# Kernel optimization log

Measured on AMD Instinct MI355X. Metric: run time of the kernel, lower is better.

The kernel has to match this reference:

```python
import jax, jax.numpy as jnp
import numpy as np

B, H, S, DH = 8, 16, 512, 64
HID = H * DH


def setup_inputs() -> dict:
    key = jax.random.key(0)
    ks = jax.random.split(key, 16)
    # padding vectors: 1s up to a per-sample valid length, 0s afterwards
    # (first zero index == valid length, matching create_padding_matrix semantics)
    len_q = jax.random.randint(ks[0], (B,), S // 2, S + 1)
    len_k = jax.random.randint(ks[1], (B,), S // 2, S + 1)
    r = jnp.arange(S)
    pq = (r[None, :] < len_q[:, None]).astype(jnp.int32)
    pk = (r[None, :] < len_k[:, None]).astype(jnp.int32)
    sc = 0.02
    inp = {
        "padding_vector_q": pq,
        "padding_vector_k": pk,
        "query_t_1": jnp.zeros((1,), jnp.float32),
        "key_t": jnp.zeros((1,), jnp.float32),
        "hidden_states": jnp.zeros((1,), jnp.float32),
        "hidden_states_t_1": jnp.zeros((1,), jnp.float32),
        "hidden_from_last": jax.random.normal(ks[2], (B, H, S, DH), jnp.float32),
        "hidden_current": jax.random.normal(ks[3], (B, H, S, DH), jnp.float32),
        "max_n_codes": S,
        "interpretabity": 0,
        "iter_idx": 0,
        "W_v1": jax.random.normal(ks[4], (HID, HID), jnp.float32) * sc,
        "b_v1": jnp.zeros((HID,), jnp.float32),
        "W_v": jax.random.normal(ks[5], (HID, HID), jnp.float32) * sc,
        "b_v": jnp.zeros((HID,), jnp.float32),
        "W_q": jax.random.normal(ks[6], (HID, HID), jnp.float32) * sc,
        "b_q": jnp.zeros((HID,), jnp.float32),
        "W_k": jax.random.normal(ks[7], (HID, HID), jnp.float32) * sc,
        "b_k": jnp.zeros((HID,), jnp.float32),
        "W_cat": jax.random.normal(ks[8], (2 * DH, DH), jnp.float32) * sc,
        "b_cat": jnp.zeros((DH,), jnp.float32),
    }
    return inp


def reference(padding_vector_q, padding_vector_k, query_t_1, key_t,
              hidden_states, hidden_states_t_1, hidden_from_last, hidden_current,
              max_n_codes, interpretabity, iter_idx,
              W_v1, b_v1, W_v, b_v, W_q, b_q, W_k, b_k, W_cat, b_cat):
    b, h, s, dh = hidden_from_last.shape
    hid = h * dh
    # permute(0,2,1,3).flatten(start_dim=2): [B,H,S,Dh] -> [B,S,H*Dh]
    flat_last = hidden_from_last.transpose(0, 2, 1, 3).reshape(b, s, hid)
    flat_cur = hidden_current.transpose(0, 2, 1, 3).reshape(b, s, hid)

    def heads(x):  # [B,S,HID] -> [B,H,S,Dh]
        return x.reshape(b, s, h, dh).transpose(0, 2, 1, 3)

    v1 = heads(flat_last @ W_v1 + b_v1)   # value_t_1(hidden_from_last)
    vt = heads(flat_cur @ W_v + b_v)      # value(hidden_current)
    q = heads(flat_last @ W_q + b_q)
    k = heads(flat_cur @ W_k + b_k)

    scores = jnp.einsum('bhqd,bhkd->bhqk', q, k) / jnp.sqrt(jnp.float32(dh))
    scores_t = scores.transpose(0, 1, 3, 2)  # [B,H,Sk,Sq] (original permute(0,1,3,2))

    # vectorized per-sample padding mask: valid window [0:padd_q, 0:padd_k]
    def first_zero(v):
        hz = jnp.any(v == 0, axis=1)
        return jnp.where(hz, jnp.argmax(v == 0, axis=1), s)

    pq_len = first_zero(padding_vector_q)
    pk_len = first_zero(padding_vector_k)
    r = jnp.arange(s)
    valid = (r[None, :, None] < pq_len[:, None, None]) & \
            (r[None, None, :] < pk_len[:, None, None])  # [B,S,S]
    mask = (~valid)[:, None, :, :]  # True = masked, broadcast over heads

    # -1e9 underflows to exactly 0 after softmax in fp32, matching the
    # masked_fill(-inf) -> softmax -> masked_fill(0) chain without NaN rows
    NEG = jnp.float32(-1e9)
    attn = jax.nn.softmax(jnp.where(mask, NEG, scores_t), axis=-1)
    attention_values = jnp.where(mask, jnp.float32(0), attn)

    context_layer = jnp.einsum('bhks,bhsd->bhkd', attention_values, v1)
    context_layer2 = jnp.concatenate([context_layer, vt], axis=-1) @ W_cat + b_cat
    return attention_values, scores_t, context_layer2, context_layer
```

## Files before the change

kernel.cpp:

```cpp
#include <hip/hip_runtime.h>
#include <cstddef>

#define NB 8
#define NH 16
#define NS 512
#define NDH 64
#define NHID 1024
#define NBH (NB*NH)

#define QKV_ELEMS (NB*NH*NS*NDH)
#define ATTN_ELEMS ((size_t)NB*NH*(size_t)NS*NS)

typedef __bf16 bf16;
typedef __attribute__((ext_vector_type(8))) __bf16 bf16x8;
typedef __attribute__((ext_vector_type(4))) __bf16 bf16x4;
typedef __attribute__((ext_vector_type(4))) float f32x4;
typedef unsigned int u32;

__device__ __forceinline__ void gload_lds16(const void* g, void* l) {
    __builtin_amdgcn_global_load_lds(
        (const __attribute__((address_space(1))) u32*)g,
        (__attribute__((address_space(3))) u32*)l, 16, 0, 0);
}

__device__ __forceinline__ int swz(int idx, int row) { return idx ^ ((row & 7) << 3); }

__global__ void lens_kernel(const int* __restrict__ pq, const int* __restrict__ pk,
                            int* __restrict__ lens) {
    int bi = blockIdx.x;
    const int* v = (bi < NB) ? pq : pk;
    int b = bi & (NB - 1);
    int lane = threadIdx.x;
    int local = NS;
#pragma unroll
    for (int p = 0; p < NS / 64; ++p) {
        int idx = p * 64 + lane;
        if (v[b * NS + idx] == 0 && idx < local) local = idx;
    }
#pragma unroll
    for (int m = 32; m >= 1; m >>= 1) {
        int o = __shfl_xor(local, m, 64);
        local = min(local, o);
    }
    if (lane == 0) lens[bi] = local;
}

__global__ __launch_bounds__(256) void cvtA_kernel(
    const float* __restrict__ hl, const float* __restrict__ hc,
    bf16* __restrict__ al, bf16* __restrict__ ac) {
    const float* src = blockIdx.z ? hc : hl;
    bf16* dst = blockIdx.z ? ac : al;
    int tid = blockIdx.x * 256 + threadIdx.x;
    int d8 = tid & 7, s = (tid >> 3) & 511, h = (tid >> 12) & 15, b = tid >> 16;
    const float* p = &src[(((size_t)b * NH + h) * NS + s) * NDH + d8 * 8];
    float4 v0 = *(const float4*)p;
    float4 v1 = *(const float4*)(p + 4);
    bf16x8 o;
    o[0] = (bf16)v0.x; o[1] = (bf16)v0.y; o[2] = (bf16)v0.z; o[3] = (bf16)v0.w;
    o[4] = (bf16)v1.x; o[5] = (bf16)v1.y; o[6] = (bf16)v1.z; o[7] = (bf16)v1.w;
    *(bf16x8*)&dst[((size_t)(b * NS + s)) * NHID + h * NDH + d8 * 8] = o;
}

__global__ __launch_bounds__(256) void cvtW_kernel(
    const float* __restrict__ Wq, const float* __restrict__ Wk,
    const float* __restrict__ Wv1, const float* __restrict__ Wv,
    bf16* __restrict__ Wt) {
    const float* W;
    switch (blockIdx.z) {
        case 0: W = Wq; break;
        case 1: W = Wk; break;
        case 2: W = Wv1; break;
        default: W = Wv; break;
    }
    bf16* out = Wt + (size_t)blockIdx.z * NHID * NHID;
    __shared__ bf16 T[64][72];
    int t = threadIdx.x;
    int k0 = blockIdx.y * 64, n0 = blockIdx.x * 64;
#pragma unroll
    for (int p = 0; p < 4; ++p) {
        int kk = p * 16 + (t >> 4), c4 = (t & 15) * 4;
        float4 v = *(const float4*)&W[(size_t)(k0 + kk) * NHID + n0 + c4];
        T[c4 + 0][kk] = (bf16)v.x;
        T[c4 + 1][kk] = (bf16)v.y;
        T[c4 + 2][kk] = (bf16)v.z;
        T[c4 + 3][kk] = (bf16)v.w;
    }
    __syncthreads();
#pragma unroll
    for (int p = 0; p < 2; ++p) {
        int f = p * 256 + t;
        int nn = f >> 3, k8 = (f & 7) * 8;
        bf16x8 o;
#pragma unroll
        for (int e = 0; e < 8; ++e) o[e] = T[nn][k8 + e];
        *(bf16x8*)&out[(size_t)(n0 + nn) * NHID + k0 + k8] = o;
    }
}

__global__ __launch_bounds__(256) void proj_kernel(
    const bf16* __restrict__ al, const bf16* __restrict__ ac,
    const bf16* __restrict__ Wt,
    const float* __restrict__ bq, const float* __restrict__ bk,
    const float* __restrict__ bv1, const float* __restrict__ bv,
    bf16* __restrict__ oq, bf16* __restrict__ ok,
    bf16* __restrict__ ov1, bf16* __restrict__ ovt) {
    __shared__ bf16 As[128 * 64];
    __shared__ bf16 Bs[128 * 64];
    const bf16* A; const bf16* W; const float* bias; bf16* dst;
    switch (blockIdx.z) {
        case 0: A = al; W = Wt;                 bias = bq;  dst = oq;  break;
        case 1: A = ac; W = Wt + 1048576;       bias = bk;  dst = ok;  break;
        case 2: A = al; W = Wt + 2097152;       bias = bv1; dst = ov1; break;
        default: A = ac; W = Wt + 3145728;      bias = bv;  dst = ovt; break;
    }
    int t = threadIdx.x, lane = t & 63, w = t >> 6;
    int wm = w & 1, wn = w >> 1;
    int m0 = blockIdx.y * 128, n0 = blockIdx.x * 128;
    int lrow = lane >> 3, lk8 = (lane & 7) * 8;
    f32x4 acc[4][4];
#pragma unroll
    for (int i = 0; i < 4; ++i)
#pragma unroll
        for (int j = 0; j < 4; ++j) acc[i][j] = (f32x4){0.f, 0.f, 0.f, 0.f};

    for (int kb = 0; kb < NHID; kb += 64) {
#pragma unroll
        for (int i = 0; i < 4; ++i) {
            int seg = w * 2048 + i * 512;
            int row = (w * 32 + i * 8) + lrow;
            gload_lds16(&A[(size_t)(m0 + row) * NHID + kb + lk8], &As[seg]);
            gload_lds16(&W[(size_t)(n0 + row) * NHID + kb + lk8], &Bs[seg]);
        }
        __syncthreads();
#pragma unroll
        for (int ks = 0; ks < 2; ++ks) {
            int ko = ks * 32 + (lane >> 4) * 8;
            bf16x8 a[4], bb[4];
#pragma unroll
            for (int i = 0; i < 4; ++i)
                a[i] = *(const bf16x8*)&As[(wm * 64 + i * 16 + (lane & 15)) * 64 + ko];
#pragma unroll
            for (int j = 0; j < 4; ++j)
                bb[j] = *(const bf16x8*)&Bs[(wn * 64 + j * 16 + (lane & 15)) * 64 + ko];
#pragma unroll
            for (int i = 0; i < 4; ++i)
#pragma unroll
                for (int j = 0; j < 4; ++j)
                    acc[i][j] = __builtin_amdgcn_mfma_f32_16x16x32_bf16(a[i], bb[j], acc[i][j], 0, 0, 0);
        }
        __syncthreads();
    }
    float bsv[4];
#pragma unroll
    for (int j = 0; j < 4; ++j) bsv[j] = bias[n0 + wn * 64 + j * 16 + (lane & 15)];
#pragma unroll
    for (int i = 0; i < 4; ++i)
#pragma unroll
        for (int r = 0; r < 4; ++r) {
            int m = m0 + wm * 64 + i * 16 + (lane >> 4) * 4 + r;
            int b = m >> 9, s = m & (NS - 1);
#pragma unroll
            for (int j = 0; j < 4; ++j) {
                int n = n0 + wn * 64 + j * 16 + (lane & 15);
                dst[(((size_t)b * NH + (n >> 6)) * NS + s) * NDH + (n & 63)] =
                    (bf16)(acc[i][j][r] + bsv[j]);
            }
        }
}

__global__ __launch_bounds__(256) void attn_kernel(
    const bf16* __restrict__ qb, const bf16* __restrict__ kb,
    const int* __restrict__ lens,
    float* __restrict__ scores, float* __restrict__ attn) {
    __shared__ bf16 Ks[64 * 64];
    __shared__ float redm[4][64];
    __shared__ float reds[4][64];
    int bh = blockIdx.y, ki0 = blockIdx.x * 64;
    int b = bh >> 4;
    int t = threadIdx.x, lane = t & 63, w = t >> 6;
    int lq = lens[b], lk = lens[NB + b];
    const bf16* kbb = kb + ((size_t)bh * NS + ki0) * NDH;
    const bf16* qbb = qb + (size_t)bh * NS * NDH;
#pragma unroll
    for (int p = 0; p < 2; ++p) {
        int f = p * 256 + t;
        int row = f >> 3, d8 = (f & 7) * 8;
        bf16x8 v = *(const bf16x8*)&kbb[(size_t)row * NDH + d8];
        *(bf16x8*)&Ks[swz(row * 64 + d8, row)] = v;
    }
    __syncthreads();
    f32x4 acc[4][8];
#pragma unroll
    for (int i = 0; i < 4; ++i)
#pragma unroll
        for (int j = 0; j < 8; ++j) acc[i][j] = (f32x4){0.f, 0.f, 0.f, 0.f};
#pragma unroll
    for (int ds = 0; ds < 2; ++ds) {
        int kofs = ds * 32 + (lane >> 4) * 8;
        bf16x8 a[4];
#pragma unroll
        for (int i = 0; i < 4; ++i) {
            int row = i * 16 + (lane & 15);
            a[i] = *(const bf16x8*)&Ks[swz(row * 64 + kofs, row)];
        }
#pragma unroll
        for (int j = 0; j < 8; ++j) {
            int qi = w * 128 + j * 16 + (lane & 15);
            bf16x8 bq8 = *(const bf16x8*)&qbb[(size_t)qi * NDH + kofs];
#pragma unroll
            for (int i = 0; i < 4; ++i)
                acc[i][j] = __builtin_amdgcn_mfma_f32_16x16x32_bf16(a[i], bq8, acc[i][j], 0, 0, 0);
        }
    }
    int g = lane >> 4, c = lane & 15;
    float pmax[4][4];
#pragma unroll
    for (int i = 0; i < 4; ++i)
#pragma unroll
        for (int r = 0; r < 4; ++r) pmax[i][r] = -3.0e38f;
#pragma unroll
    for (int i = 0; i < 4; ++i)
#pragma unroll
        for (int j = 0; j < 8; ++j) {
            int qi = w * 128 + j * 16 + c;
            bool colv = qi < lk;
#pragma unroll
            for (int r = 0; r < 4; ++r) {
                float s = acc[i][j][r] * 0.125f;
                acc[i][j][r] = s;
                scores[((size_t)bh * NS + ki0 + i * 16 + g * 4 + r) * NS + qi] = s;
                if (colv) pmax[i][r] = fmaxf(pmax[i][r], s);
            }
        }
#pragma unroll
    for (int msk = 8; msk >= 1; msk >>= 1)
#pragma unroll
        for (int i = 0; i < 4; ++i)
#pragma unroll
            for (int r = 0; r < 4; ++r)
                pmax[i][r] = fmaxf(pmax[i][r], __shfl_xor(pmax[i][r], msk, 64));
    if (c == 0)
#pragma unroll
        for (int i = 0; i < 4; ++i)
#pragma unroll
            for (int r = 0; r < 4; ++r) redm[w][i * 16 + g * 4 + r] = pmax[i][r];
    __syncthreads();
    float rmax[4][4];
#pragma unroll
    for (int i = 0; i < 4; ++i)
#pragma unroll
        for (int r = 0; r < 4; ++r) {
            int row = i * 16 + g * 4 + r;
            rmax[i][r] = fmaxf(fmaxf(redm[0][row], redm[1][row]),
                               fmaxf(redm[2][row], redm[3][row]));
        }
    float psum[4][4];
#pragma unroll
    for (int i = 0; i < 4; ++i)
#pragma unroll
        for (int r = 0; r < 4; ++r) psum[i][r] = 0.f;
#pragma unroll
    for (int i = 0; i < 4; ++i)
#pragma unroll
        for (int j = 0; j < 8; ++j) {
            int qi = w * 128 + j * 16 + c;
            bool colv = qi < lk;
#pragma unroll
            for (int r = 0; r < 4; ++r) {
                float e = colv ? __expf(acc[i][j][r] - rmax[i][r]) : 0.f;
                acc[i][j][r] = e;
                psum[i][r] += e;
            }
        }
#pragma unroll
    for (int msk = 8; msk >= 1; msk >>= 1)
#pragma unroll
        for (int i = 0; i < 4; ++i)
#pragma unroll
            for (int r = 0; r < 4; ++r)
                psum[i][r] += __shfl_xor(psum[i][r], msk, 64);
    if (c == 0)
#pragma unroll
        for (int i = 0; i < 4; ++i)
#pragma unroll
            for (int r = 0; r < 4; ++r) reds[w][i * 16 + g * 4 + r] = psum[i][r];
    __syncthreads();
#pragma unroll
    for (int i = 0; i < 4; ++i)
#pragma unroll
        for (int r = 0; r < 4; ++r) {
            int row = i * 16 + g * 4 + r;
            float rs = reds[0][row] + reds[1][row] + reds[2][row] + reds[3][row];
            float inv = (rs > 0.f) ? 1.f / rs : 0.f;
            bool rowv = (ki0 + row) < lq;
#pragma unroll
            for (int j = 0; j < 8; ++j) {
                int qi = w * 128 + j * 16 + c;
                float v = rowv ? acc[i][j][r] * inv : 0.f;
                attn[((size_t)bh * NS + ki0 + row) * NS + qi] = v;
            }
        }
}

__global__ __launch_bounds__(256) void context_kernel(
    const float* __restrict__ attn, const bf16* __restrict__ v1,
    float* __restrict__ ctx) {
    __shared__ bf16 Ash[64 * 64];
    __shared__ bf16 Vs[64 * 64];
    int bh = blockIdx.y, ki0 = blockIdx.x * 64;
    int t = threadIdx.x, lane = t & 63, w = t >> 6;
    const float* ab = attn + ((size_t)bh * NS + ki0) * NS;
    const bf16* vb = v1 + (size_t)bh * NS * NDH;
    f32x4 acc[4];
#pragma unroll
    for (int j = 0; j < 4; ++j) acc[j] = (f32x4){0.f, 0.f, 0.f, 0.f};

    for (int q0 = 0; q0 < NS; q0 += 64) {
#pragma unroll
        for (int p = 0; p < 4; ++p) {
            int f = p * 256 + t;
            int row = f >> 4, c4 = (f & 15) * 4;
            float4 v = *(const float4*)&ab[(size_t)row * NS + q0 + c4];
            bf16x4 h;
            h[0] = (bf16)v.x; h[1] = (bf16)v.y; h[2] = (bf16)v.z; h[3] = (bf16)v.w;
            *(bf16x4*)&Ash[swz(row * 64 + c4, row)] = h;
        }
#pragma unroll
        for (int p = 0; p < 2; ++p) {
            int f = p * 256 + t;
            int qr = f >> 3, d8 = (f & 7) * 8;
            bf16x8 v = *(const bf16x8*)&vb[(size_t)(q0 + qr) * NDH + d8];
#pragma unroll
            for (int e = 0; e < 8; ++e) {
                int d = d8 + e;
                Vs[swz(d * 64 + qr, d)] = v[e];
            }
        }
        __syncthreads();
#pragma unroll
        for (int kk = 0; kk < 2; ++kk) {
            int kofs = kk * 32 + (lane >> 4) * 8;
            int arow = w * 16 + (lane & 15);
            bf16x8 a = *(const bf16x8*)&Ash[swz(arow * 64 + kofs, arow)];
#pragma unroll
            for (int j = 0; j < 4; ++j) {
                int d = j * 16 + (lane & 15);
                bf16x8 bv8 = *(const bf16x8*)&Vs[swz(d * 64 + kofs, d)];
                acc[j] = __builtin_amdgcn_mfma_f32_16x16x32_bf16(a, bv8, acc[j], 0, 0, 0);
            }
        }
        __syncthreads();
    }
    int g = lane >> 4, c = lane & 15;
#pragma unroll
    for (int j = 0; j < 4; ++j)
#pragma unroll
        for (int r = 0; r < 4; ++r) {
            int ki = ki0 + w * 16 + g * 4 + r;
            ctx[((size_t)bh * NS + ki) * NDH + j * 16 + c] = acc[j][r];
        }
}

__global__ __launch_bounds__(256) void cat_kernel(
    const float* __restrict__ ctx, const bf16* __restrict__ vt,
    const float* __restrict__ Wcat, const float* __restrict__ bcat,
    float* __restrict__ out) {
    __shared__ float As[16][68];
    __shared__ float Bs[16][68];
    int t = threadIdx.x;
    int tx = t & 15, ty = t >> 4;
    int row0 = blockIdx.x * 64;
    float acc[4][4];
#pragma unroll
    for (int i = 0; i < 4; ++i)
#pragma unroll
        for (int j = 0; j < 4; ++j) acc[i][j] = 0.f;

    for (int k0 = 0; k0 < 2 * NDH; k0 += 16) {
#pragma unroll
        for (int p = 0; p < 4; ++p) {
            int e = p * 256 + t;
            int kk = e & 15, mm = e >> 4;
            int cidx = k0 + kk;
            float val = (cidx < NDH) ? ctx[(size_t)(row0 + mm) * NDH + cidx]
                                     : (float)vt[(size_t)(row0 + mm) * NDH + (cidx - NDH)];
            As[kk][mm] = val;
        }
#pragma unroll
        for (int p = 0; p < 4; ++p) {
            int e = p * 256 + t;
            int nn = e & 63, kk = e >> 6;
            Bs[kk][nn] = Wcat[(size_t)(k0 + kk) * NDH + nn];
        }
        __syncthreads();
#pragma unroll
        for (int kk = 0; kk < 16; ++kk) {
            float a[4], bb[4];
            *(float4*)&a[0]  = *(const float4*)&As[kk][ty * 4];
            *(float4*)&bb[0] = *(const float4*)&Bs[kk][tx * 4];
#pragma unroll
            for (int i = 0; i < 4; ++i)
#pragma unroll
                for (int j = 0; j < 4; ++j) acc[i][j] += a[i] * bb[j];
        }
        __syncthreads();
    }
#pragma unroll
    for (int i = 0; i < 4; ++i) {
        int n = tx * 4;
        float4 o;
        o.x = acc[i][0] + bcat[n + 0];
        o.y = acc[i][1] + bcat[n + 1];
        o.z = acc[i][2] + bcat[n + 2];
        o.w = acc[i][3] + bcat[n + 3];
        *(float4*)&out[(size_t)(row0 + ty * 4 + i) * NDH + n] = o;
    }
}

extern "C" void kernel_launch(void* const* d_in, const int* in_sizes, int n_in,
                              void* d_out, int out_size, void* d_ws, size_t ws_size,
                              hipStream_t stream) {
    (void)in_sizes; (void)n_in; (void)out_size; (void)ws_size;
    const int*   pq   = (const int*)d_in[0];
    const int*   pk   = (const int*)d_in[1];
    const float* hl   = (const float*)d_in[6];
    const float* hc   = (const float*)d_in[7];
    const float* Wv1  = (const float*)d_in[11];
    const float* bv1  = (const float*)d_in[12];
    const float* Wv   = (const float*)d_in[13];
    const float* bv   = (const float*)d_in[14];
    const float* Wq   = (const float*)d_in[15];
    const float* bq   = (const float*)d_in[16];
    const float* Wk   = (const float*)d_in[17];
    const float* bk   = (const float*)d_in[18];
    const float* Wcat = (const float*)d_in[19];
    const float* bcat = (const float*)d_in[20];

    float* out_attn   = (float*)d_out;
    float* out_scores = out_attn + ATTN_ELEMS;
    float* out_ctx2   = out_attn + 2 * ATTN_ELEMS;
    float* out_ctx    = out_ctx2 + QKV_ELEMS;

    char* ws = (char*)d_ws;
    bf16* al   = (bf16*)(ws);
    bf16* acb  = (bf16*)(ws + 8388608);
    bf16* WtB  = (bf16*)(ws + 16777216);
    bf16* qb   = (bf16*)(ws + 25165824);
    bf16* kbp  = (bf16*)(ws + 33554432);
    bf16* v1b  = (bf16*)(ws + 41943040);
    bf16* vtb  = (bf16*)(ws + 50331648);
    int*  lens = (int*)(ws + 58720256);

    lens_kernel<<<16, 64, 0, stream>>>(pq, pk, lens);
    cvtA_kernel<<<dim3(2048, 1, 2), 256, 0, stream>>>(hl, hc, al, acb);
    cvtW_kernel<<<dim3(16, 16, 4), 256, 0, stream>>>(Wq, Wk, Wv1, Wv, WtB);
    proj_kernel<<<dim3(8, 32, 4), 256, 0, stream>>>(
        al, acb, WtB, bq, bk, bv1, bv, qb, kbp, v1b, vtb);
    attn_kernel<<<dim3(8, NBH), 256, 0, stream>>>(qb, kbp, lens, out_scores, out_attn);
    context_kernel<<<dim3(8, NBH), 256, 0, stream>>>(out_attn, v1b, out_ctx);
    cat_kernel<<<(NB * NH * NS) / 64, 256, 0, stream>>>(out_ctx, vtb, Wcat, bcat, out_ctx2);
}
```

Baseline: 512.5 us.

## Fuse context matmul into attention kernel, reusing probabilities from registers

Merges the separate context kernel into the attention kernel. Softmax probabilities held in registers are staged as bf16 in shared memory, one wave's 128-column slice per pass, and multiplied with V1 tiles, so the fp32 attention matrix no longer has to be re-read from global memory. Key chunks beyond the valid key length are skipped, and fully masked row blocks just write zero context. The cost is more shared memory, which may lower occupancy, plus extra barriers and serialized per-wave staging.

```diff
diff --git a/kernel.cpp b/kernel.cpp
--- a/kernel.cpp
+++ b/kernel.cpp
@@ -168,11 +168,14 @@
         }
 }
 
-__global__ __launch_bounds__(256) void attn_kernel(
+__global__ __launch_bounds__(256) void attn_fused_kernel(
     const bf16* __restrict__ qb, const bf16* __restrict__ kb,
-    const int* __restrict__ lens,
-    float* __restrict__ scores, float* __restrict__ attn) {
+    const bf16* __restrict__ v1, const int* __restrict__ lens,
+    float* __restrict__ scores, float* __restrict__ attn,
+    float* __restrict__ ctx) {
     __shared__ bf16 Ks[64 * 64];
+    __shared__ bf16 Ps[64 * 128];
+    __shared__ bf16 Vs[64 * 128];
     __shared__ float redm[4][64];
     __shared__ float reds[4][64];
     int bh = blockIdx.y, ki0 = blockIdx.x * 64;
@@ -181,6 +184,7 @@
     int lq = lens[b], lk = lens[NB + b];
     const bf16* kbb = kb + ((size_t)bh * NS + ki0) * NDH;
     const bf16* qbb = qb + (size_t)bh * NS * NDH;
+    const bf16* vb  = v1 + (size_t)bh * NS * NDH;
 #pragma unroll
     for (int p = 0; p < 2; ++p) {
         int f = p * 256 + t;
@@ -293,71 +297,73 @@
             float rs = reds[0][row] + reds[1][row] + reds[2][row] + reds[3][row];
             float inv = (rs > 0.f) ? 1.f / rs : 0.f;
             bool rowv = (ki0 + row) < lq;
+            float fin = rowv ? inv : 0.f;
 #pragma unroll
             for (int j = 0; j < 8; ++j) {
                 int qi = w * 128 + j * 16 + c;
-                float v = rowv ? acc[i][j][r] * inv : 0.f;
+                float v = acc[i][j][r] * fin;
+                acc[i][j][r] = v;
                 attn[((size_t)bh * NS + ki0 + row) * NS + qi] = v;
             }
         }
-}
-
-__global__ __launch_bounds__(256) void context_kernel(
-    const float* __restrict__ attn, const bf16* __restrict__ v1,
-    float* __restrict__ ctx) {
-    __shared__ bf16 Ash[64 * 64];
-    __shared__ bf16 Vs[64 * 64];
-    int bh = blockIdx.y, ki0 = blockIdx.x * 64;
-    int t = threadIdx.x, lane = t & 63, w = t >> 6;
-    const float* ab = attn + ((size_t)bh * NS + ki0) * NS;
-    const bf16* vb = v1 + (size_t)bh * NS * NDH;
-    f32x4 acc[4];
-#pragma unroll
-    for (int j = 0; j < 4; ++j) acc[j] = (f32x4){0.f, 0.f, 0.f, 0.f};
-
-    for (int q0 = 0; q0 < NS; q0 += 64) {
+    if (ki0 >= lq) {
 #pragma unroll
         for (int p = 0; p < 4; ++p) {
             int f = p * 256 + t;
             int row = f >> 4, c4 = (f & 15) * 4;
-            float4 v = *(const float4*)&ab[(size_t)row * NS + q0 + c4];
-            bf16x4 h;
-            h[0] = (bf16)v.x; h[1] = (bf16)v.y; h[2] = (bf16)v.z; h[3] = (bf16)v.w;
-            *(bf16x4*)&Ash[swz(row * 64 + c4, row)] = h;
-        }
-#pragma unroll
-        for (int p = 0; p < 2; ++p) {
+            *(float4*)&ctx[((size_t)bh * NS + ki0 + row) * NDH + c4] =
+                make_float4(0.f, 0.f, 0.f, 0.f);
+        }
+        return;
+    }
+    f32x4 cacc[4];
+#pragma unroll
+    for (int j = 0; j < 4; ++j) cacc[j] = (f32x4){0.f, 0.f, 0.f, 0.f};
+    for (int cq = 0; cq < 4; ++cq) {
+        if (cq * 128 >= lk) break;
+        __syncthreads();
+#pragma unroll
+        for (int p = 0; p < 4; ++p) {
             int f = p * 256 + t;
             int qr = f >> 3, d8 = (f & 7) * 8;
-            bf16x8 v = *(const bf16x8*)&vb[(size_t)(q0 + qr) * NDH + d8];
-#pragma unroll
-            for (int e = 0; e < 8; ++e) {
-                int d = d8 + e;
-                Vs[swz(d * 64 + qr, d)] = v[e];
-            }
-        }
-        __syncthreads();
-#pragma unroll
-        for (int kk = 0; kk < 2; ++kk) {
-            int kofs = kk * 32 + (lane >> 4) * 8;
+            bf16x8 v = *(const bf16x8*)&vb[(size_t)(cq * 128 + qr) * NDH + d8];
+#pragma unroll
+            for (int e = 0; e < 8; ++e)
+                Vs[swz((d8 + e) * 128 + qr, d8 + e)] = v[e];
+        }
+        if (w == cq) {
+#pragma unroll
+            for (int i = 0; i < 4; ++i)
+#pragma unroll
+                for (int j = 0; j < 8; ++j) {
+                    int qc = j * 16 + c;
+#pragma unroll
+                    for (int r = 0; r < 4; ++r) {
+                        int row = i * 16 + g * 4 + r;
+                        Ps[swz(row * 128 + qc, row)] = (bf16)acc[i][j][r];
+                    }
+                }
+        }
+        __syncthreads();
+#pragma unroll
+        for (int ks = 0; ks < 4; ++ks) {
+            int kofs = ks * 32 + (lane >> 4) * 8;
             int arow = w * 16 + (lane & 15);
-            bf16x8 a = *(const bf16x8*)&Ash[swz(arow * 64 + kofs, arow)];
+            bf16x8 a = *(const bf16x8*)&Ps[swz(arow * 128 + kofs, arow)];
 #pragma unroll
             for (int j = 0; j < 4; ++j) {
                 int d = j * 16 + (lane & 15);
-                bf16x8 bv8 = *(const bf16x8*)&Vs[swz(d * 64 + kofs, d)];
-                acc[j] = __builtin_amdgcn_mfma_f32_16x16x32_bf16(a, bv8, acc[j], 0, 0, 0);
+                bf16x8 bv8 = *(const bf16x8*)&Vs[swz(d * 128 + kofs, d)];
+                cacc[j] = __builtin_amdgcn_mfma_f32_16x16x32_bf16(a, bv8, cacc[j], 0, 0, 0);
             }
         }
-        __syncthreads();
-    }
-    int g = lane >> 4, c = lane & 15;
+    }
 #pragma unroll
     for (int j = 0; j < 4; ++j)
 #pragma unroll
         for (int r = 0; r < 4; ++r) {
             int ki = ki0 + w * 16 + g * 4 + r;
-            ctx[((size_t)bh * NS + ki) * NDH + j * 16 + c] = acc[j][r];
+            ctx[((size_t)bh * NS + ki) * NDH + j * 16 + c] = cacc[j][r];
         }
 }
 
@@ -456,7 +462,7 @@
     cvtW_kernel<<<dim3(16, 16, 4), 256, 0, stream>>>(Wq, Wk, Wv1, Wv, WtB);
     proj_kernel<<<dim3(8, 32, 4), 256, 0, stream>>>(
         al, acb, WtB, bq, bk, bv1, bv, qb, kbp, v1b, vtb);
-    attn_kernel<<<dim3(8, NBH), 256, 0, stream>>>(qb, kbp, lens, out_scores, out_attn);
-    context_kernel<<<dim3(8, NBH), 256, 0, stream>>>(out_attn, v1b, out_ctx);
+    attn_fused_kernel<<<dim3(8, NBH), 256, 0, stream>>>(
+        qb, kbp, v1b, lens, out_scores, out_attn, out_ctx);
     cat_kernel<<<(NB * NH * NS) / 64, 256, 0, stream>>>(out_ctx, vtb, Wcat, bcat, out_ctx2);
 }
```

New measurement: 495.9 us. 3.2% less time.
